# Optimization experiments

Measured on AMD Instinct MI355X. Metric: run time of the kernel, lower is better.

## Reference

```python
import jax, jax.numpy as jnp
import numpy as np

N_HEAD = 16
N_KV_HEAD = 8
HEAD_DIM = 128
BLOCK_SIZE = 2048


def _rope_cache(T, hd):
    # faithful to torch: freqs repeat_interleave(2) along last dim
    inv_freq = 1.0 / (10000.0 ** (jnp.arange(0, hd, 2, dtype=jnp.float32) / hd))
    t = jnp.arange(T, dtype=jnp.float32)
    freqs = jnp.outer(t, inv_freq)            # [T, hd/2]
    freqs = jnp.repeat(freqs, 2, axis=-1)     # [T, hd]
    return jnp.cos(freqs), jnp.sin(freqs)


def _apply_rope(x, cos, sin):
    # x: [B, H, T, hd]; rotate-half convention from the torch code
    hd = x.shape[-1]
    x1, x2 = x[..., : hd // 2], x[..., hd // 2 :]
    x_rot = jnp.concatenate([-x2, x1], axis=-1)
    return x * cos + x_rot * sin


def setup_inputs() -> dict:
    key = jax.random.key(0)
    ks = jax.random.split(key, 5)
    B, T, C = 4, 2048, 2048
    kv_dim = N_KV_HEAD * HEAD_DIM
    s = 0.02
    return {
        "x": jax.random.normal(ks[0], (B, T, C), dtype=jnp.float32),
        "Wq": jax.random.normal(ks[1], (C, C), dtype=jnp.float32) * s,
        "Wk": jax.random.normal(ks[2], (kv_dim, C), dtype=jnp.float32) * s,
        "Wv": jax.random.normal(ks[3], (kv_dim, C), dtype=jnp.float32) * s,
        "Wo": jax.random.normal(ks[4], (C, C), dtype=jnp.float32) * s,
    }


def reference(x, Wq, Wk, Wv, Wo):
    B, T, C = x.shape
    hd = HEAD_DIM
    # projections (torch Linear: x @ W.T)
    q = (x @ Wq.T).reshape(B, T, N_HEAD, hd).transpose(0, 2, 1, 3)      # [B,H,T,hd]
    k = (x @ Wk.T).reshape(B, T, N_KV_HEAD, hd).transpose(0, 2, 1, 3)   # [B,Hkv,T,hd]
    v = (x @ Wv.T).reshape(B, T, N_KV_HEAD, hd).transpose(0, 2, 1, 3)

    cos, sin = _rope_cache(T, hd)  # start_pos = 0
    q = _apply_rope(q, cos, sin)
    k = _apply_rope(k, cos, sin)

    # GQA: repeat kv heads
    rep = N_HEAD // N_KV_HEAD
    k = jnp.repeat(k, rep, axis=1)  # [B,H,T,hd]
    v = jnp.repeat(v, rep, axis=1)

    scale = 1.0 / jnp.sqrt(jnp.float32(hd))
    scores = jnp.einsum("bhqd,bhkd->bhqk", q, k) * scale
    causal = jnp.tril(jnp.ones((T, T), dtype=bool))
    scores = jnp.where(causal, scores, jnp.finfo(scores.dtype).min)
    attn = jax.nn.softmax(scores, axis=-1)
    out = jnp.einsum("bhqk,bhkd->bhqd", attn, v)  # [B,H,T,hd]

    y = out.transpose(0, 2, 1, 3).reshape(B, T, C)
    return y @ Wo.T
```

## Files before the change

kernel.cpp:

```cpp
#include <hip/hip_runtime.h>

#define SCALE 0.08838834764831845f

typedef unsigned short bfu;
typedef __attribute__((ext_vector_type(8))) short bf16x8;
typedef __attribute__((ext_vector_type(4))) float f32x4;
typedef __attribute__((ext_vector_type(16))) float f32x16;

__device__ __forceinline__ unsigned short f2bf(float f) {
  unsigned int u = __float_as_uint(f);
  u += 0x7FFFu + ((u >> 16) & 1u);
  return (unsigned short)(u >> 16);
}
__device__ __forceinline__ float bf2f(unsigned short h) {
  return __uint_as_float(((unsigned int)h) << 16);
}
__device__ __forceinline__ unsigned int cvtpk(float a, float b) {
  unsigned int r;
  asm("v_cvt_pk_bf16_f32 %0, %1, %2" : "=v"(r) : "v"(a), "v"(b));
  return r;
}
__device__ __forceinline__ void async16(const void* g, void* l) {
  __builtin_amdgcn_global_load_lds(
      (const __attribute__((address_space(1))) unsigned int*)g,
      (__attribute__((address_space(3))) unsigned int*)l, 16, 0, 0);
}
__device__ __forceinline__ void barrier_sb() {
  __builtin_amdgcn_sched_barrier(0);
  __builtin_amdgcn_s_barrier();
  __builtin_amdgcn_sched_barrier(0);
}
__device__ __forceinline__ void wait4_bar() {
  __builtin_amdgcn_sched_barrier(0);
  asm volatile("s_waitcnt vmcnt(4)" ::: "memory");
  __builtin_amdgcn_s_barrier();
  __builtin_amdgcn_sched_barrier(0);
}
__device__ __forceinline__ void wait0_bar() {
  __builtin_amdgcn_sched_barrier(0);
  asm volatile("s_waitcnt vmcnt(0)" ::: "memory");
  __builtin_amdgcn_s_barrier();
  __builtin_amdgcn_sched_barrier(0);
}

__global__ __launch_bounds__(256) void cvt_bf16(const float* __restrict__ src,
                                                bfu* __restrict__ dst, int n4) {
  int i = blockIdx.x * 256 + threadIdx.x;
  if (i >= n4) return;
  float4 v = ((const float4*)src)[i];
  ushort4 o;
  o.x = f2bf(v.x); o.y = f2bf(v.y); o.z = f2bf(v.z); o.w = f2bf(v.w);
  ((ushort4*)dst)[i] = o;
}

__device__ __forceinline__ void storeC(float* p, float v) { *p = v; }
__device__ __forceinline__ void storeC(bfu* p, float v) { *p = f2bf(v); }

template <typename OutT>
__global__ __launch_bounds__(512, 2) void gemm256(const bfu* __restrict__ A,
                                                  const bfu* __restrict__ B,
                                                  OutT* __restrict__ C,
                                                  int M, int N, int K) {
  __shared__ __align__(16) char smem[131072];
  const int tid = threadIdx.x;
  const int w = tid >> 6, l = tid & 63;
  const int lr = l & 15, lg = l >> 4;
  const int wr = w >> 2, wc = w & 3;

  const int nwg = gridDim.x * gridDim.y;
  const int flat = blockIdx.y * gridDim.x + blockIdx.x;
  const int swz = (flat & 7) * (nwg >> 3) + (flat >> 3);
  const int m0 = (swz % gridDim.x) * 256;
  const int n0 = (swz / gridDim.x) * 256;

  const int sr = l >> 3;
  const int sc = (l & 7) ^ sr;
  auto stageHalf = [&](const bfu* G, int grow0, int kcol, char* lds) {
#pragma unroll
    for (int j = 0; j < 2; j++) {
      int row = (j * 8 + w) * 8 + sr;
      async16(G + (size_t)(grow0 + row) * K + kcol + sc * 8,
              lds + (j * 8 + w) * 1024 + l * 16);
    }
  };

  f32x4 acc[8][4];
#pragma unroll
  for (int i = 0; i < 8; i++)
#pragma unroll
    for (int j = 0; j < 4; j++) acc[i][j] = (f32x4){0.f, 0.f, 0.f, 0.f};

  stageHalf(A, m0, 0, smem);
  stageHalf(A, m0 + 128, 0, smem + 16384);
  stageHalf(B, n0, 0, smem + 65536);
  stageHalf(B, n0 + 128, 0, smem + 65536 + 16384);

  const int KT = K >> 6;
  const int swiz = (lr & 7) << 4;
#pragma unroll 1
  for (int t = 0; t < KT; t++) {
    const int bt = t & 1;
    const char* Ah = smem + bt * 32768 + wr * 16384;
    const char* Bt = smem + 65536 + bt * 32768;
    char* An = smem + (bt ^ 1) * 32768;
    char* Bn = smem + 65536 + (bt ^ 1) * 32768;
    const bool pfch = (t + 1 < KT);
    const int kn = (t + 1) << 6;

    if (pfch) {
      stageHalf(A, m0, kn, An);
      asm volatile("s_waitcnt vmcnt(2)" ::: "memory");
    } else {
      asm volatile("s_waitcnt vmcnt(0)" ::: "memory");
    }
    barrier_sb();

    bf16x8 bfr[4][2];
#pragma unroll
    for (int n = 0; n < 4; n++) {
      const char* rowp = Bt + (wc * 64 + n * 16 + lr) * 128;
#pragma unroll
      for (int s = 0; s < 2; s++)
        bfr[n][s] = *(const bf16x8*)(rowp + ((((s << 2) + lg) << 4) ^ swiz));
    }

#pragma unroll
    for (int p = 0; p < 4; p++) {
      bf16x8 af[2][2];
#pragma unroll
      for (int m2 = 0; m2 < 2; m2++) {
        const char* rowp = Ah + ((p * 2 + m2) * 16 + lr) * 128;
#pragma unroll
        for (int s = 0; s < 2; s++)
          af[m2][s] = *(const bf16x8*)(rowp + ((((s << 2) + lg) << 4) ^ swiz));
      }
      if (pfch) {
        if (p == 1) stageHalf(A, m0 + 128, kn, An + 16384);
        if (p == 2) stageHalf(B, n0, kn, Bn);
        if (p == 3) stageHalf(B, n0 + 128, kn, Bn + 16384);
      }
      __builtin_amdgcn_s_setprio(1);
#pragma unroll
      for (int m2 = 0; m2 < 2; m2++)
#pragma unroll
        for (int n = 0; n < 4; n++)
#pragma unroll
          for (int s = 0; s < 2; s++)
            acc[p * 2 + m2][n] = __builtin_amdgcn_mfma_f32_16x16x32_bf16(
                af[m2][s], bfr[n][s], acc[p * 2 + m2][n], 0, 0, 0);
      __builtin_amdgcn_s_setprio(0);
    }
    barrier_sb();
  }

#pragma unroll
  for (int i = 0; i < 8; i++)
#pragma unroll
    for (int j = 0; j < 4; j++)
#pragma unroll
      for (int r = 0; r < 4; r++) {
        int gm = m0 + wr * 128 + i * 16 + lg * 4 + r;
        int gn = n0 + wc * 64 + j * 16 + lr;
        storeC(&C[(size_t)gm * N + gn], acc[i][j][r]);
      }
}

__global__ __launch_bounds__(256) void rope_kernel(const bfu* __restrict__ QKV,
                                                   bfu* __restrict__ qT,
                                                   bfu* __restrict__ kT) {
  int idx = blockIdx.x * 256 + threadIdx.x;
  int d = idx & 63;
  int tmp = idx >> 6;
  int head = tmp % 24;
  int bt = tmp / 24;
  int t = bt & 2047;
  int b = bt >> 11;
  const bfu* src;
  bfu* dst;
  if (head < 16) {
    src = QKV + (size_t)bt * 4096 + head * 128;
    dst = qT + (((size_t)(b * 16 + head)) * 2048 + t) * 128;
  } else {
    int kh = head - 16;
    src = QKV + (size_t)bt * 4096 + 2048 + kh * 128;
    dst = kT + (((size_t)(b * 8 + kh)) * 2048 + t) * 128;
  }
  float x1 = bf2f(src[d]);
  float x2 = bf2f(src[d + 64]);
  const float nl = -0.14391156463f;
  int i1 = d >> 1;
  float th1 = (float)t * expf((float)i1 * nl);
  float th2 = (float)t * expf((float)(i1 + 32) * nl);
  float c1 = cosf(th1), s1 = sinf(th1);
  float c2 = cosf(th2), s2 = sinf(th2);
  dst[d] = f2bf(x1 * c1 - x2 * s1);
  dst[d + 64] = f2bf(x2 * c2 + x1 * s2);
}

__global__ __launch_bounds__(256) void vtrans_kernel(const bfu* __restrict__ QKV,
                                                     bfu* __restrict__ vT) {
  int idx = blockIdx.x * 256 + threadIdx.x;
  int t = idx & 2047;
  int r = idx >> 11;
  int dd = r & 127;
  int khb = r >> 7;
  int kh = khb & 7;
  int b = khb >> 3;
  vT[idx] = QKV[(((size_t)(b * 2048 + t)) * 4096) + 3072 + kh * 128 + dd];
}

__global__ __launch_bounds__(256, 3) void flash_attn5(const bfu* __restrict__ qT,
                                                      const bfu* __restrict__ kT,
                                                      const bfu* __restrict__ vT,
                                                      bfu* __restrict__ attn) {
  __shared__ __align__(16) char smem[49152];
  const int tid = threadIdx.x;
  const int w = tid >> 6, l = tid & 63;
  const int ln = l & 31, h2 = l >> 5;
  const int idx = blockIdx.x;
  const int khb = idx & 31;
  const int hs = (idx >> 5) & 1;
  const int qt = 15 - (idx >> 6);
  const int kh = khb & 7, b = khb >> 3;
  const int hh = kh * 2 + hs;
  const int NT = 2 * qt + 2;
  const int qrow0 = qt * 128 + w * 32;
  const int myrow = qrow0 + ln;

  const bfu* Qh = qT + ((size_t)(b * 16 + hh) * 2048) * 128;
  const bfu* Kb = kT + ((size_t)(b * 8 + kh) * 2048) * 128;
  const bfu* Vb = vT + ((size_t)(b * 8 + kh) * 128) * 2048;

  auto stageK = [&](int kbuf, int t) {
    char* Kl = smem + kbuf * 16384;
    const bfu* src = Kb + (size_t)t * 64 * 128;
#pragma unroll
    for (int ii = 0; ii < 4; ii++) {
      int i = w * 4 + ii;
      int row = i * 4 + (l >> 4);
      int ck = (l & 15) ^ (row & 15);
      async16(src + row * 128 + ck * 8, Kl + i * 1024 + l * 16);
    }
  };
  auto stageV = [&](int t) {
    char* Vl = smem + 32768;
    const bfu* src = Vb + t * 64;
#pragma unroll
    for (int jj = 0; jj < 4; jj++) {
      int j = w * 4 + jj;
      int row = j * 8 + (l >> 3);
      int ck = (l & 7) ^ (row & 7);
      async16(src + (size_t)row * 2048 + ck * 8, Vl + j * 1024 + l * 16);
    }
  };

  bf16x8 qf[8];
#pragma unroll
  for (int dt = 0; dt < 8; dt++)
    qf[dt] = *(const bf16x8*)(Qh + (size_t)myrow * 128 + dt * 16 + h2 * 8);

  f32x16 O[4];
#pragma unroll
  for (int mt = 0; mt < 4; mt++)
#pragma unroll
    for (int r = 0; r < 16; r++) O[mt][r] = 0.f;
  float li = 0.f;

  stageK(0, 0);
  stageV(0);
  wait4_bar();

  int kb = 0;
#pragma unroll 1
  for (int t = 0; t < NT; t++) {
    const bool pf = (t + 1 < NT);
    if (pf) stageK(kb ^ 1, t + 1);

    const int k0 = t * 64;
    const bool active = k0 <= qrow0 + 31;
    bf16x8 pfr[4];

    if (active) {
      const char* Kl = smem + kb * 16384;
      f32x16 S0, S1;
#pragma unroll
      for (int r = 0; r < 16; r++) { S0[r] = 0.f; S1[r] = 0.f; }
      const int swk = (ln & 15) << 4;
      __builtin_amdgcn_s_setprio(1);
#pragma unroll
      for (int dt = 0; dt < 8; dt++) {
        bf16x8 kf0 =
            *(const bf16x8*)(Kl + ln * 256 + ((dt * 32 + h2 * 16) ^ swk));
        bf16x8 kf1 = *(const bf16x8*)(Kl + (32 + ln) * 256 +
                                      ((dt * 32 + h2 * 16) ^ swk));
        S0 = __builtin_amdgcn_mfma_f32_32x32x16_bf16(kf0, qf[dt], S0, 0, 0, 0);
        S1 = __builtin_amdgcn_mfma_f32_32x32x16_bf16(kf1, qf[dt], S1, 0, 0, 0);
      }
      __builtin_amdgcn_s_setprio(0);

      const bool need_mask = (k0 + 63) > qrow0;
#pragma unroll
      for (int half = 0; half < 2; half++) {
        float p[16];
#pragma unroll
        for (int r = 0; r < 16; r++) {
          float s = half ? S1[r] : S0[r];
          float pv = __builtin_exp2f(fmaf(s, 0.12751743f, -17.312340f));
          if (need_mask) {
            int key = k0 + half * 32 + (r & 3) + 8 * (r >> 2) + 4 * h2;
            if (key > myrow) pv = 0.f;
          }
          p[r] = pv;
          li += pv;
        }
#pragma unroll
        for (int kt = 0; kt < 2; kt++) {
          const float* q = p + kt * 8;
          unsigned int lo0 = cvtpk(q[0], q[1]);
          unsigned int lo1 = cvtpk(q[2], q[3]);
          unsigned int hi0 = cvtpk(q[4], q[5]);
          unsigned int hi1 = cvtpk(q[6], q[7]);
          unsigned int plo0 = __shfl_xor((int)lo0, 32);
          unsigned int plo1 = __shfl_xor((int)lo1, 32);
          unsigned int phi0 = __shfl_xor((int)hi0, 32);
          unsigned int phi1 = __shfl_xor((int)hi1, 32);
          union { unsigned int u[4]; bf16x8 v; } c;
          c.u[0] = h2 ? phi0 : lo0;
          c.u[1] = h2 ? phi1 : lo1;
          c.u[2] = h2 ? hi0 : plo0;
          c.u[3] = h2 ? hi1 : plo1;
          pfr[half * 2 + kt] = c.v;
        }
      }
    }

    if (pf) wait4_bar(); else wait0_bar();

    if (active) {
      const char* Vl = smem + 32768;
      const int swv = (ln & 7) << 4;
      __builtin_amdgcn_s_setprio(1);
#pragma unroll
      for (int mt = 0; mt < 4; mt++) {
        const char* vb = Vl + (mt * 32 + ln) * 128;
#pragma unroll
        for (int kt = 0; kt < 4; kt++) {
          bf16x8 vf = *(const bf16x8*)(vb + ((kt * 32 + h2 * 16) ^ swv));
          O[mt] = __builtin_amdgcn_mfma_f32_32x32x16_bf16(vf, pfr[kt], O[mt], 0, 0, 0);
        }
      }
      __builtin_amdgcn_s_setprio(0);
    }

    if (pf) {
      wait0_bar();
      stageV(t + 1);
    }
    kb ^= 1;
  }

  li += __shfl_xor(li, 32);
  const float inv = 1.f / li;
  bfu* orow = attn + ((size_t)(b * 2048 + qrow0 + ln)) * 2048 + hh * 128;
#pragma unroll
  for (int mt = 0; mt < 4; mt++)
#pragma unroll
    for (int g = 0; g < 4; g++) {
      unsigned int r0 = cvtpk(O[mt][g * 4 + 0] * inv, O[mt][g * 4 + 1] * inv);
      unsigned int r1 = cvtpk(O[mt][g * 4 + 2] * inv, O[mt][g * 4 + 3] * inv);
      uint2 o; o.x = r0; o.y = r1;
      *(uint2*)(orow + mt * 32 + g * 8 + h2 * 4) = o;
    }
}

extern "C" void kernel_launch(void* const* d_in, const int* in_sizes, int n_in,
                              void* d_out, int out_size, void* d_ws, size_t ws_size,
                              hipStream_t stream) {
  const float* x = (const float*)d_in[0];
  const float* Wq = (const float*)d_in[1];
  const float* Wk = (const float*)d_in[2];
  const float* Wv = (const float*)d_in[3];
  const float* Wo = (const float*)d_in[4];
  float* out = (float*)d_out;
  char* ws = (char*)d_ws;

  bfu* xb   = (bfu*)(ws);
  bfu* Wqkv = (bfu*)(ws + 33554432);
  bfu* Wob  = (bfu*)(ws + 50331648);
  bfu* QKV  = (bfu*)(ws + 58720256);
  bfu* qT   = (bfu*)(ws + 125829120);
  bfu* kT   = (bfu*)(ws + 159383552);
  bfu* vT   = (bfu*)(ws + 176160768);
  bfu* attn = xb;

  cvt_bf16<<<16384, 256, 0, stream>>>(x, xb, 4194304);
  cvt_bf16<<<4096, 256, 0, stream>>>(Wq, Wqkv, 1048576);
  cvt_bf16<<<2048, 256, 0, stream>>>(Wk, Wqkv + (size_t)2048 * 2048, 524288);
  cvt_bf16<<<2048, 256, 0, stream>>>(Wv, Wqkv + (size_t)3072 * 2048, 524288);
  cvt_bf16<<<4096, 256, 0, stream>>>(Wo, Wob, 1048576);

  gemm256<bfu><<<dim3(32, 16), 512, 0, stream>>>(xb, Wqkv, QKV, 8192, 4096, 2048);
  rope_kernel<<<49152, 256, 0, stream>>>(QKV, qT, kT);
  vtrans_kernel<<<32768, 256, 0, stream>>>(QKV, vT);
  flash_attn5<<<1024, 256, 0, stream>>>(qT, kT, vT, attn);
  gemm256<float><<<dim3(32, 8), 512, 0, stream>>>(attn, Wob, out, 8192, 2048, 2048);
}
```

Measured before the change: 551.6 us.

## Halve flash-attention KV tile to 32 keys for higher occupancy, use permlane32 swap

Shrinks the per-iteration key/value tile from 64 to 32 keys, halving shared memory (48KB to 24KB) and raising the occupancy hint from 3 to 5 blocks per CU. The LDS swizzle patterns for K and V are redesigned for the narrower tiles. The cross-half-wave exchange of P fragments now uses v_permlane32_swap instead of four ds shuffles plus selects. The trade-off is twice as many loop iterations, each with its own barriers and wait points, and less MFMA work to hide latency per iteration.

```diff
diff --git a/kernel.cpp b/kernel.cpp
--- a/kernel.cpp
+++ b/kernel.cpp
@@ -20,6 +20,9 @@
   asm("v_cvt_pk_bf16_f32 %0, %1, %2" : "=v"(r) : "v"(a), "v"(b));
   return r;
 }
+__device__ __forceinline__ void pl32swap(unsigned int& a, unsigned int& b) {
+  asm volatile("v_permlane32_swap_b32 %0, %1" : "+v"(a), "+v"(b));
+}
 __device__ __forceinline__ void async16(const void* g, void* l) {
   __builtin_amdgcn_global_load_lds(
       (const __attribute__((address_space(1))) unsigned int*)g,
@@ -30,9 +33,9 @@
   __builtin_amdgcn_s_barrier();
   __builtin_amdgcn_sched_barrier(0);
 }
-__device__ __forceinline__ void wait4_bar() {
-  __builtin_amdgcn_sched_barrier(0);
-  asm volatile("s_waitcnt vmcnt(4)" ::: "memory");
+__device__ __forceinline__ void wait2_bar() {
+  __builtin_amdgcn_sched_barrier(0);
+  asm volatile("s_waitcnt vmcnt(2)" ::: "memory");
   __builtin_amdgcn_s_barrier();
   __builtin_amdgcn_sched_barrier(0);
 }
@@ -209,11 +212,11 @@
   vT[idx] = QKV[(((size_t)(b * 2048 + t)) * 4096) + 3072 + kh * 128 + dd];
 }
 
-__global__ __launch_bounds__(256, 3) void flash_attn5(const bfu* __restrict__ qT,
+__global__ __launch_bounds__(256, 5) void flash_attn6(const bfu* __restrict__ qT,
                                                       const bfu* __restrict__ kT,
                                                       const bfu* __restrict__ vT,
                                                       bfu* __restrict__ attn) {
-  __shared__ __align__(16) char smem[49152];
+  __shared__ __align__(16) char smem[24576];
   const int tid = threadIdx.x;
   const int w = tid >> 6, l = tid & 63;
   const int ln = l & 31, h2 = l >> 5;
@@ -223,7 +226,7 @@
   const int qt = 15 - (idx >> 6);
   const int kh = khb & 7, b = khb >> 3;
   const int hh = kh * 2 + hs;
-  const int NT = 2 * qt + 2;
+  const int NT = 4 * qt + 4;
   const int qrow0 = qt * 128 + w * 32;
   const int myrow = qrow0 + ln;
 
@@ -232,25 +235,25 @@
   const bfu* Vb = vT + ((size_t)(b * 8 + kh) * 128) * 2048;
 
   auto stageK = [&](int kbuf, int t) {
-    char* Kl = smem + kbuf * 16384;
-    const bfu* src = Kb + (size_t)t * 64 * 128;
-#pragma unroll
-    for (int ii = 0; ii < 4; ii++) {
-      int i = w * 4 + ii;
+    char* Kl = smem + kbuf * 8192;
+    const bfu* src = Kb + (size_t)t * 32 * 128;
+#pragma unroll
+    for (int ii = 0; ii < 2; ii++) {
+      int i = w * 2 + ii;
       int row = i * 4 + (l >> 4);
-      int ck = (l & 15) ^ (row & 15);
-      async16(src + row * 128 + ck * 8, Kl + i * 1024 + l * 16);
+      int s = (row + (row >> 3)) & 15;
+      async16(src + row * 128 + ((l & 15) ^ s) * 8, Kl + i * 1024 + l * 16);
     }
   };
   auto stageV = [&](int t) {
-    char* Vl = smem + 32768;
-    const bfu* src = Vb + t * 64;
-#pragma unroll
-    for (int jj = 0; jj < 4; jj++) {
-      int j = w * 4 + jj;
-      int row = j * 8 + (l >> 3);
-      int ck = (l & 7) ^ (row & 7);
-      async16(src + (size_t)row * 2048 + ck * 8, Vl + j * 1024 + l * 16);
+    char* Vl = smem + 16384;
+    const bfu* src = Vb + t * 32;
+#pragma unroll
+    for (int jj = 0; jj < 2; jj++) {
+      int j = w * 2 + jj;
+      int row = j * 16 + (l >> 2);
+      int c = (l & 3) ^ ((l >> 3) & 3);
+      async16(src + (size_t)row * 2048 + c * 8, Vl + j * 1024 + l * 16);
     }
   };
 
@@ -268,83 +271,71 @@
 
   stageK(0, 0);
   stageV(0);
-  wait4_bar();
-
+  wait2_bar();
+
+  const int skb = ((ln + (ln >> 3)) & 15) << 4;
+  const int swv = ((ln >> 1) & 3) << 4;
   int kb = 0;
 #pragma unroll 1
   for (int t = 0; t < NT; t++) {
     const bool pf = (t + 1 < NT);
     if (pf) stageK(kb ^ 1, t + 1);
 
-    const int k0 = t * 64;
+    const int k0 = t * 32;
     const bool active = k0 <= qrow0 + 31;
-    bf16x8 pfr[4];
+    bf16x8 pfr[2];
 
     if (active) {
-      const char* Kl = smem + kb * 16384;
-      f32x16 S0, S1;
-#pragma unroll
-      for (int r = 0; r < 16; r++) { S0[r] = 0.f; S1[r] = 0.f; }
-      const int swk = (ln & 15) << 4;
+      const char* Kl = smem + kb * 8192;
+      f32x16 S0;
+#pragma unroll
+      for (int r = 0; r < 16; r++) S0[r] = 0.f;
       __builtin_amdgcn_s_setprio(1);
 #pragma unroll
       for (int dt = 0; dt < 8; dt++) {
-        bf16x8 kf0 =
-            *(const bf16x8*)(Kl + ln * 256 + ((dt * 32 + h2 * 16) ^ swk));
-        bf16x8 kf1 = *(const bf16x8*)(Kl + (32 + ln) * 256 +
-                                      ((dt * 32 + h2 * 16) ^ swk));
-        S0 = __builtin_amdgcn_mfma_f32_32x32x16_bf16(kf0, qf[dt], S0, 0, 0, 0);
-        S1 = __builtin_amdgcn_mfma_f32_32x32x16_bf16(kf1, qf[dt], S1, 0, 0, 0);
+        bf16x8 kf =
+            *(const bf16x8*)(Kl + ln * 256 + ((((dt << 1) + h2) << 4) ^ skb));
+        S0 = __builtin_amdgcn_mfma_f32_32x32x16_bf16(kf, qf[dt], S0, 0, 0, 0);
       }
       __builtin_amdgcn_s_setprio(0);
 
-      const bool need_mask = (k0 + 63) > qrow0;
-#pragma unroll
-      for (int half = 0; half < 2; half++) {
-        float p[16];
-#pragma unroll
-        for (int r = 0; r < 16; r++) {
-          float s = half ? S1[r] : S0[r];
-          float pv = __builtin_exp2f(fmaf(s, 0.12751743f, -17.312340f));
-          if (need_mask) {
-            int key = k0 + half * 32 + (r & 3) + 8 * (r >> 2) + 4 * h2;
-            if (key > myrow) pv = 0.f;
-          }
-          p[r] = pv;
-          li += pv;
+      const bool need_mask = (k0 + 31) > qrow0;
+      float p[16];
+#pragma unroll
+      for (int r = 0; r < 16; r++) {
+        float pv = __builtin_exp2f(fmaf(S0[r], 0.12751743f, -17.312340f));
+        if (need_mask) {
+          int key = k0 + (r & 3) + 8 * (r >> 2) + 4 * h2;
+          if (key > myrow) pv = 0.f;
         }
+        p[r] = pv;
+        li += pv;
+      }
+#pragma unroll
+      for (int kt = 0; kt < 2; kt++) {
+        const float* q = p + kt * 8;
+        unsigned int a0 = cvtpk(q[0], q[1]);
+        unsigned int a1 = cvtpk(q[2], q[3]);
+        unsigned int b0 = cvtpk(q[4], q[5]);
+        unsigned int b1 = cvtpk(q[6], q[7]);
+        pl32swap(a0, b0);
+        pl32swap(a1, b1);
+        union { unsigned int u[4]; bf16x8 v; } c;
+        c.u[0] = a0; c.u[1] = a1; c.u[2] = b0; c.u[3] = b1;
+        pfr[kt] = c.v;
+      }
+    }
+
+    if (pf) wait2_bar(); else wait0_bar();
+
+    if (active) {
+      const char* Vl = smem + 16384;
+      __builtin_amdgcn_s_setprio(1);
+#pragma unroll
+      for (int mt = 0; mt < 4; mt++) {
+        const char* vb = Vl + (mt * 32 + ln) * 64;
 #pragma unroll
         for (int kt = 0; kt < 2; kt++) {
-          const float* q = p + kt * 8;
-          unsigned int lo0 = cvtpk(q[0], q[1]);
-          unsigned int lo1 = cvtpk(q[2], q[3]);
-          unsigned int hi0 = cvtpk(q[4], q[5]);
-          unsigned int hi1 = cvtpk(q[6], q[7]);
-          unsigned int plo0 = __shfl_xor((int)lo0, 32);
-          unsigned int plo1 = __shfl_xor((int)lo1, 32);
-          unsigned int phi0 = __shfl_xor((int)hi0, 32);
-          unsigned int phi1 = __shfl_xor((int)hi1, 32);
-          union { unsigned int u[4]; bf16x8 v; } c;
-          c.u[0] = h2 ? phi0 : lo0;
-          c.u[1] = h2 ? phi1 : lo1;
-          c.u[2] = h2 ? hi0 : plo0;
-          c.u[3] = h2 ? hi1 : plo1;
-          pfr[half * 2 + kt] = c.v;
-        }
-      }
-    }
-
-    if (pf) wait4_bar(); else wait0_bar();
-
-    if (active) {
-      const char* Vl = smem + 32768;
-      const int swv = (ln & 7) << 4;
-      __builtin_amdgcn_s_setprio(1);
-#pragma unroll
-      for (int mt = 0; mt < 4; mt++) {
-        const char* vb = Vl + (mt * 32 + ln) * 128;
-#pragma unroll
-        for (int kt = 0; kt < 4; kt++) {
           bf16x8 vf = *(const bf16x8*)(vb + ((kt * 32 + h2 * 16) ^ swv));
           O[mt] = __builtin_amdgcn_mfma_f32_32x32x16_bf16(vf, pfr[kt], O[mt], 0, 0, 0);
         }
@@ -402,6 +393,6 @@
   gemm256<bfu><<<dim3(32, 16), 512, 0, stream>>>(xb, Wqkv, QKV, 8192, 4096, 2048);
   rope_kernel<<<49152, 256, 0, stream>>>(QKV, qT, kT);
   vtrans_kernel<<<32768, 256, 0, stream>>>(QKV, vT);
-  flash_attn5<<<1024, 256, 0, stream>>>(qT, kT, vT, attn);
+  flash_attn6<<<1024, 256, 0, stream>>>(qT, kT, vT, attn);
   gemm256<float><<<dim3(32, 8), 512, 0, stream>>>(attn, Wob, out, 8192, 2048, 2048);
 }
```

After: 780.3 us. +41.5%, slower.

## Fuse RoPE and V transpose into QKV GEMM epilogue with precomputed table

Applied to the files above, without the earlier changes.

The QKV projection GEMM now applies RoPE and writes Q/K directly in head-major layout. It also writes V transposed, so the separate rope and vtrans kernels and the intermediate QKV buffer are removed. The B-fragment column mapping is remapped so each wave holds both halves (d and d+64) of a head for the rotation. A small kernel precomputes a cos/sin table instead of evaluating transcendentals per element. The trade-off is scattered 2-byte stores in the GEMM epilogue and extra table reads.

```diff
diff --git a/kernel.cpp b/kernel.cpp
--- a/kernel.cpp
+++ b/kernel.cpp
@@ -53,14 +53,23 @@
   ((ushort4*)dst)[i] = o;
 }
 
+__global__ __launch_bounds__(256) void rope_table(float2* __restrict__ tab) {
+  int idx = blockIdx.x * 256 + threadIdx.x;
+  int t = idx >> 6, f = idx & 63;
+  const float nl = -0.14391156463f;
+  float th = (float)t * expf((float)f * nl);
+  tab[idx] = make_float2(cosf(th), sinf(th));
+}
+
 __device__ __forceinline__ void storeC(float* p, float v) { *p = v; }
 __device__ __forceinline__ void storeC(bfu* p, float v) { *p = f2bf(v); }
 
-template <typename OutT>
-__global__ __launch_bounds__(512, 2) void gemm256(const bfu* __restrict__ A,
-                                                  const bfu* __restrict__ B,
-                                                  OutT* __restrict__ C,
-                                                  int M, int N, int K) {
+template <typename OutT, bool FUSE>
+__global__ __launch_bounds__(512, 2) void gemm256(
+    const bfu* __restrict__ A, const bfu* __restrict__ B,
+    OutT* __restrict__ C, const float2* __restrict__ ropeTab,
+    bfu* __restrict__ qTo, bfu* __restrict__ kTo, bfu* __restrict__ vTo,
+    int M, int N, int K) {
   __shared__ __align__(16) char smem[131072];
   const int tid = threadIdx.x;
   const int w = tid >> 6, l = tid & 63;
@@ -97,6 +106,7 @@
 
   const int KT = K >> 6;
   const int swiz = (lr & 7) << 4;
+  const int cbase = (wc >> 1) * 128 + (wc & 1) * 32;
 #pragma unroll 1
   for (int t = 0; t < KT; t++) {
     const int bt = t & 1;
@@ -118,7 +128,8 @@
     bf16x8 bfr[4][2];
 #pragma unroll
     for (int n = 0; n < 4; n++) {
-      const char* rowp = Bt + (wc * 64 + n * 16 + lr) * 128;
+      const char* rowp =
+          Bt + (cbase + (n & 1) * 16 + (n >> 1) * 64 + lr) * 128;
 #pragma unroll
       for (int s = 0; s < 2; s++)
         bfr[n][s] = *(const bf16x8*)(rowp + ((((s << 2) + lg) << 4) ^ swiz));
@@ -153,60 +164,61 @@
     barrier_sb();
   }
 
-#pragma unroll
-  for (int i = 0; i < 8; i++)
-#pragma unroll
-    for (int j = 0; j < 4; j++)
-#pragma unroll
-      for (int r = 0; r < 4; r++) {
-        int gm = m0 + wr * 128 + i * 16 + lg * 4 + r;
-        int gn = n0 + wc * 64 + j * 16 + lr;
-        storeC(&C[(size_t)gm * N + gn], acc[i][j][r]);
-      }
-}
-
-__global__ __launch_bounds__(256) void rope_kernel(const bfu* __restrict__ QKV,
-                                                   bfu* __restrict__ qT,
-                                                   bfu* __restrict__ kT) {
-  int idx = blockIdx.x * 256 + threadIdx.x;
-  int d = idx & 63;
-  int tmp = idx >> 6;
-  int head = tmp % 24;
-  int bt = tmp / 24;
-  int t = bt & 2047;
-  int b = bt >> 11;
-  const bfu* src;
-  bfu* dst;
-  if (head < 16) {
-    src = QKV + (size_t)bt * 4096 + head * 128;
-    dst = qT + (((size_t)(b * 16 + head)) * 2048 + t) * 128;
+  if constexpr (!FUSE) {
+#pragma unroll
+    for (int i = 0; i < 8; i++)
+#pragma unroll
+      for (int j = 0; j < 4; j++)
+#pragma unroll
+        for (int r = 0; r < 4; r++) {
+          int gm = m0 + wr * 128 + i * 16 + lg * 4 + r;
+          int gn = n0 + cbase + (j & 1) * 16 + (j >> 1) * 64 + lr;
+          storeC(&C[(size_t)gm * N + gn], acc[i][j][r]);
+        }
   } else {
-    int kh = head - 16;
-    src = QKV + (size_t)bt * 4096 + 2048 + kh * 128;
-    dst = kT + (((size_t)(b * 8 + kh)) * 2048 + t) * 128;
+    const int head = (n0 >> 7) + (wc >> 1);
+    if (head < 24) {
+#pragma unroll
+      for (int i = 0; i < 8; i++)
+#pragma unroll
+        for (int r = 0; r < 4; r++) {
+          int gm = m0 + wr * 128 + i * 16 + lg * 4 + r;
+          int tt = gm & 2047, bb = gm >> 11;
+          bfu* rowp = (head < 16)
+                          ? qTo + (((size_t)((bb * 16 + head) * 2048 + tt)) << 7)
+                          : kTo + (((size_t)((bb * 8 + head - 16) * 2048 + tt)) << 7);
+          const float2* trow = ropeTab + tt * 64;
+#pragma unroll
+          for (int n = 0; n < 2; n++) {
+            int d = (wc & 1) * 32 + n * 16 + lr;
+            int i1 = d >> 1;
+            float2 cs1 = trow[i1];
+            float2 cs2 = trow[i1 + 32];
+            float x1 = acc[i][n][r], x2 = acc[i][n + 2][r];
+            rowp[d] = f2bf(x1 * cs1.x - x2 * cs1.y);
+            rowp[d + 64] = f2bf(x2 * cs2.x + x1 * cs2.y);
+          }
+        }
+    } else {
+      const int kh = head - 24;
+#pragma unroll
+      for (int i = 0; i < 8; i++) {
+        int gm0 = m0 + wr * 128 + i * 16 + lg * 4;
+        int t0 = gm0 & 2047, bb = gm0 >> 11;
+#pragma unroll
+        for (int n = 0; n < 4; n++) {
+          int d = (wc & 1) * 32 + (n & 1) * 16 + (n >> 1) * 64 + lr;
+          bfu* p = vTo + (((size_t)((bb * 8 + kh) * 128 + d)) << 11) + t0;
+          ushort4 o;
+          o.x = f2bf(acc[i][n][0]);
+          o.y = f2bf(acc[i][n][1]);
+          o.z = f2bf(acc[i][n][2]);
+          o.w = f2bf(acc[i][n][3]);
+          *(ushort4*)p = o;
+        }
+      }
+    }
   }
-  float x1 = bf2f(src[d]);
-  float x2 = bf2f(src[d + 64]);
-  const float nl = -0.14391156463f;
-  int i1 = d >> 1;
-  float th1 = (float)t * expf((float)i1 * nl);
-  float th2 = (float)t * expf((float)(i1 + 32) * nl);
-  float c1 = cosf(th1), s1 = sinf(th1);
-  float c2 = cosf(th2), s2 = sinf(th2);
-  dst[d] = f2bf(x1 * c1 - x2 * s1);
-  dst[d + 64] = f2bf(x2 * c2 + x1 * s2);
-}
-
-__global__ __launch_bounds__(256) void vtrans_kernel(const bfu* __restrict__ QKV,
-                                                     bfu* __restrict__ vT) {
-  int idx = blockIdx.x * 256 + threadIdx.x;
-  int t = idx & 2047;
-  int r = idx >> 11;
-  int dd = r & 127;
-  int khb = r >> 7;
-  int kh = khb & 7;
-  int b = khb >> 3;
-  vT[idx] = QKV[(((size_t)(b * 2048 + t)) * 4096) + 3072 + kh * 128 + dd];
 }
 
 __global__ __launch_bounds__(256, 3) void flash_attn5(const bfu* __restrict__ qT,
@@ -384,13 +396,13 @@
   float* out = (float*)d_out;
   char* ws = (char*)d_ws;
 
-  bfu* xb   = (bfu*)(ws);
-  bfu* Wqkv = (bfu*)(ws + 33554432);
-  bfu* Wob  = (bfu*)(ws + 50331648);
-  bfu* QKV  = (bfu*)(ws + 58720256);
-  bfu* qT   = (bfu*)(ws + 125829120);
-  bfu* kT   = (bfu*)(ws + 159383552);
-  bfu* vT   = (bfu*)(ws + 176160768);
+  bfu* xb     = (bfu*)(ws);
+  bfu* Wqkv   = (bfu*)(ws + 33554432);
+  bfu* Wob    = (bfu*)(ws + 50331648);
+  float2* tab = (float2*)(ws + 58720256);
+  bfu* qT     = (bfu*)(ws + 125829120);
+  bfu* kT     = (bfu*)(ws + 159383552);
+  bfu* vT     = (bfu*)(ws + 176160768);
   bfu* attn = xb;
 
   cvt_bf16<<<16384, 256, 0, stream>>>(x, xb, 4194304);
@@ -398,10 +410,11 @@
   cvt_bf16<<<2048, 256, 0, stream>>>(Wk, Wqkv + (size_t)2048 * 2048, 524288);
   cvt_bf16<<<2048, 256, 0, stream>>>(Wv, Wqkv + (size_t)3072 * 2048, 524288);
   cvt_bf16<<<4096, 256, 0, stream>>>(Wo, Wob, 1048576);
-
-  gemm256<bfu><<<dim3(32, 16), 512, 0, stream>>>(xb, Wqkv, QKV, 8192, 4096, 2048);
-  rope_kernel<<<49152, 256, 0, stream>>>(QKV, qT, kT);
-  vtrans_kernel<<<32768, 256, 0, stream>>>(QKV, vT);
+  rope_table<<<512, 256, 0, stream>>>(tab);
+
+  gemm256<bfu, true><<<dim3(32, 16), 512, 0, stream>>>(
+      xb, Wqkv, (bfu*)nullptr, tab, qT, kT, vT, 8192, 4096, 2048);
   flash_attn5<<<1024, 256, 0, stream>>>(qT, kT, vT, attn);
-  gemm256<float><<<dim3(32, 8), 512, 0, stream>>>(attn, Wob, out, 8192, 2048, 2048);
-}
+  gemm256<float, false><<<dim3(32, 8), 512, 0, stream>>>(
+      attn, Wob, out, nullptr, nullptr, nullptr, nullptr, 8192, 2048, 2048);
+}
```

After: 488.9 us. -11.4%, faster.
